# Kernel optimization log

Hardware: AMD Instinct MI355X
Metric: run time of the kernel (lower is better)

The kernel has to match this reference:

```python
import jax, jax.numpy as jnp
import numpy as np

N = 50000      # node_num
C = 64         # num_classes
G = 3          # number of metapath graphs (len(g))
E = 1200000    # edges per metapath graph
L = 2          # layers (PLPConv propagation steps)
D = 256        # input feature dim (feat_dims[0])
H = 256        # hidden_dim


def setup_inputs() -> dict:
    key = jax.random.key(0)
    ks = jax.random.split(key, 13)
    features0 = jax.random.normal(ks[0], (N, D), jnp.float32)
    labels = jax.random.randint(ks[1], (N,), 0, C)
    labels_one_hot = jax.nn.one_hot(labels, C, dtype=jnp.float32)
    # label_init: soft labels, rows on the simplex
    label_init = jax.nn.softmax(jax.random.normal(ks[2], (N, C), jnp.float32), axis=-1)
    train_mask = (jax.random.uniform(ks[3], (N, 1)) < 0.5).astype(jnp.float32)
    src = jax.random.randint(ks[4], (G, E), 0, N, dtype=jnp.int32)
    dst = jax.random.randint(ks[5], (G, E), 0, N, dtype=jnp.int32)
    # per-layer, per-graph learned edge logits (xavier-ish small init)
    e_edges = 0.1 * jax.random.normal(ks[6], (L, G, E), jnp.float32)
    attention = 0.5 * jax.random.normal(ks[7], (N, G), jnp.float32)
    alpha = 0.5 * jax.random.normal(ks[8], (N, 1), jnp.float32)
    W1 = jax.random.normal(ks[9], (D, H), jnp.float32) / np.sqrt(D)
    b1 = jnp.zeros((H,), jnp.float32)
    W2 = jax.random.normal(ks[10], (H, C), jnp.float32) / np.sqrt(H)
    b2 = jnp.zeros((C,), jnp.float32)
    return {"features0": features0, "label_init": label_init,
            "labels_one_hot": labels_one_hot, "train_mask": train_mask,
            "src": src, "dst": dst, "e_edges": e_edges,
            "attention": attention, "alpha": alpha,
            "W1": W1, "b1": b1, "W2": W2, "b2": b2}


def _edge_softmax(e, dst, n):
    # softmax of per-edge scalar over incoming edges of each dst node
    m = jax.ops.segment_max(e, dst, num_segments=n)
    a = jnp.exp(e - m[dst])
    s = jax.ops.segment_sum(a, dst, num_segments=n)
    return a / s[dst]


def reference(features0, label_init, labels_one_hot, train_mask,
              src, dst, e_edges, attention, alpha, W1, b1, W2, b2):
    n = label_init.shape[0]
    masked_label = 1.0 - train_mask            # (~masked).float(), [N,1]
    masked_oh = labels_one_hot * train_mask    # labels_one_hot * masked, [N,C]

    # Label propagation over each metapath graph (PLPConv stack, activation=None)
    h_prime = []
    for i in range(G):
        h = label_init
        for l in range(L):
            a = _edge_softmax(e_edges[l, i], dst[i], n)         # [E]
            msg = h[src[i]] * a[:, None]                        # gather-mul [E,C]
            h = jax.ops.segment_sum(msg, dst[i], num_segments=n)  # scatter-sum [N,C]
            h = h * masked_label + masked_oh                    # clamp train labels
        h_prime.append(h)
    x = jnp.stack(h_prime, axis=-1)                             # [N,C,G]

    att_mp = jax.nn.softmax(attention, axis=1)                  # [N,G]
    logits_lp = jnp.einsum('ncg,ng->nc', x, att_mp)             # [N,C]

    # MLP2 (2 layers, dropout=0): relu(x W1 + b1) W2 + b2
    hm = jax.nn.relu(features0 @ W1 + b1)
    logits_ns = hm @ W2 + b2                                    # [N,C]

    logits = jax.nn.sigmoid(alpha) * logits_lp + jax.nn.sigmoid(-alpha) * logits_ns
    return (logits, logits_lp, logits_ns)
```

## Files before the change

kernel.cpp:

```cpp
#include <hip/hip_runtime.h>
#include <hip/hip_bf16.h>

#define NN 50000
#define CC 64
#define GG 3
#define EE 1200000
#define LL 2
#define DD 256
#define HH 256
#define NB 196
#define NBLK 293
#define NBK (GG * NB)
#define BKCAP 8192


__device__ __forceinline__ ushort f2bf(float f) {
    unsigned b = __float_as_uint(f);
    return (ushort)((b + 0x7fffu + ((b >> 16) & 1u)) >> 16);
}
__device__ __forceinline__ float bf2f(unsigned u) {
    return __uint_as_float(u << 16);
}

typedef __attribute__((ext_vector_type(8))) short s8v;
typedef __attribute__((ext_vector_type(4))) float f4v;

template<int NWM, int NWN, bool A_FP32, bool OUT_RELU_BF16>
__global__ __launch_bounds__(256) void mfma_gemm_kernel(
    const void* __restrict__ Av, const ushort* __restrict__ Bt,
    const float* __restrict__ bias, void* __restrict__ Cv, int M, int Nc)
{
    static_assert(NWM * NWN == 4, "4 waves per block");
    const int tid = threadIdx.x;
    const int w = tid >> 6;
    const int l = tid & 63;
    const int wm = w / NWN;
    const int wn = w % NWN;
    const int r0 = blockIdx.x * (NWM * 64) + wm * 64;
    const int c0 = blockIdx.y * (NWN * 64) + wn * 64;
    const int lrow = l & 15;
    const int lk = (l >> 4) << 3;

    f4v acc[4][4] = {};

    for (int k0 = 0; k0 < 256; k0 += 32) {
        s8v a[4], b[4];
        #pragma unroll
        for (int i = 0; i < 4; i++) {
            int row = r0 + lrow + 16 * i;
            row = (row < M) ? row : (M - 1);
            if constexpr (A_FP32) {
                const float* Af = (const float*)Av;
                const float4* p = (const float4*)(Af + (size_t)row * 256 + k0 + lk);
                float4 f0 = p[0], f1 = p[1];
                union { ushort u[8]; s8v v; } t;
                t.u[0] = f2bf(f0.x); t.u[1] = f2bf(f0.y);
                t.u[2] = f2bf(f0.z); t.u[3] = f2bf(f0.w);
                t.u[4] = f2bf(f1.x); t.u[5] = f2bf(f1.y);
                t.u[6] = f2bf(f1.z); t.u[7] = f2bf(f1.w);
                a[i] = t.v;
            } else {
                const ushort* Ab = (const ushort*)Av;
                a[i] = *(const s8v*)(Ab + (size_t)row * 256 + k0 + lk);
            }
        }
        #pragma unroll
        for (int j = 0; j < 4; j++) {
            int col = c0 + lrow + 16 * j;
            b[j] = *(const s8v*)(Bt + (size_t)col * 256 + k0 + lk);
        }
        #pragma unroll
        for (int i = 0; i < 4; i++)
            #pragma unroll
            for (int j = 0; j < 4; j++)
                acc[i][j] = __builtin_amdgcn_mfma_f32_16x16x32_bf16(
                    a[i], b[j], acc[i][j], 0, 0, 0);
    }

    #pragma unroll
    for (int i = 0; i < 4; i++) {
        #pragma unroll
        for (int r = 0; r < 4; r++) {
            int row = r0 + 16 * i + (l >> 4) * 4 + r;
            if (row >= M) continue;
            #pragma unroll
            for (int j = 0; j < 4; j++) {
                int col = c0 + 16 * j + lrow;
                float v = acc[i][j][r] + bias[col];
                if constexpr (OUT_RELU_BF16) {
                    v = fmaxf(v, 0.f);
                    ((ushort*)Cv)[(size_t)row * Nc + col] = f2bf(v);
                } else {
                    ((float*)Cv)[(size_t)row * Nc + col] = v;
                }
            }
        }
    }
}

__global__ void wcvt_kernel(const float* __restrict__ W1,
                            const float* __restrict__ W2,
                            ushort* __restrict__ Wt1, ushort* __restrict__ Wt2)
{
    int idx = blockIdx.x * 256 + threadIdx.x;
    if (idx < 256 * 256) {
        int n = idx >> 8, k = idx & 255;
        Wt1[idx] = f2bf(W1[k * 256 + n]);
    } else {
        int i = idx - 256 * 256;
        if (i < 64 * 256) {
            int n = i >> 8, k = i & 255;
            Wt2[i] = f2bf(W2[k * 64 + n]);
        }
    }
}

__global__ void cvt_kernel(const float* __restrict__ in, ushort* __restrict__ out, int n4)
{
    int i = blockIdx.x * blockDim.x + threadIdx.x;
    if (i >= n4) return;
    float4 f = ((const float4*)in)[i];
    ushort4 u;
    u.x = f2bf(f.x); u.y = f2bf(f.y); u.z = f2bf(f.z); u.w = f2bf(f.w);
    ((ushort4*)out)[i] = u;
}

__global__ __launch_bounds__(256) void bhist_kernel(
    const int* __restrict__ dst, int* __restrict__ bcnt)
{
    int blk = blockIdx.x;
    int g = blk / NBLK;
    int bi = blk - g * NBLK;
    int base = bi * 4096;
    __shared__ int cnt[NB];
    int t = threadIdx.x;
    if (t < NB) cnt[t] = 0;
    __syncthreads();
    #pragma unroll
    for (int k = 0; k < 16; k++) {
        int e = base + k * 256 + t;
        if (e < EE) atomicAdd(&cnt[dst[g * EE + e] >> 8], 1);
    }
    __syncthreads();
    if (t < NB && cnt[t] > 0) atomicAdd(&bcnt[g * NB + t], cnt[t]);
}

__global__ void scan_bucket(const int* __restrict__ bcnt, int* __restrict__ bs)
{
    __shared__ int sd[256];
    __shared__ int s_run;
    int t = threadIdx.x;
    if (t == 0) s_run = 0;
    __syncthreads();
    for (int base = 0; base < NBK; base += 256) {
        int i = base + t;
        int v = (i < NBK) ? bcnt[i] : 0;
        sd[t] = v;
        __syncthreads();
        for (int o = 1; o < 256; o <<= 1) {
            int x = (t >= o) ? sd[t - o] : 0;
            __syncthreads();
            sd[t] += x;
            __syncthreads();
        }
        int run = s_run;
        __syncthreads();
        if (i < NBK) bs[i] = run + sd[t] - v;
        if (t == 255) s_run = run + sd[255];
        __syncthreads();
    }
    if (t == 0) bs[NBK] = GG * EE;
}

__global__ __launch_bounds__(256) void binA_kernel(
    const int* __restrict__ dst, const int* __restrict__ src,
    const float* __restrict__ e_edges, const int* __restrict__ bucket_start,
    int* __restrict__ fill, uint2* __restrict__ staging)
{
    int blk = blockIdx.x;
    int g = blk / NBLK;
    int bi = blk - g * NBLK;
    int base = bi * 4096;
    __shared__ int cnt[NB];
    __shared__ int cur[NB];
    __shared__ int rbase[NB];
    int t = threadIdx.x;
    if (t < NB) cnt[t] = 0;
    __syncthreads();

    int myd[16];
    #pragma unroll
    for (int k = 0; k < 16; k++) {
        int e = base + k * 256 + t;
        int d = (e < EE) ? dst[g * EE + e] : -1;
        myd[k] = d;
        if (d >= 0) atomicAdd(&cnt[d >> 8], 1);
    }
    __syncthreads();
    if (t < NB) {
        int c = cnt[t];
        int b = (c > 0) ? atomicAdd(&fill[g * NB + t], c) : 0;
        rbase[t] = bucket_start[g * NB + t];
        cur[t] = b;
    }
    __syncthreads();
    #pragma unroll
    for (int k = 0; k < 16; k++) {
        int d = myd[k];
        if (d >= 0) {
            int e = base + k * 256 + t;
            int bucket = d >> 8;
            int pos = rbase[bucket] + atomicAdd(&cur[bucket], 1);
            int idxg = g * EE + e;
            uint2 rec;
            rec.x = ((unsigned)f2bf(e_edges[idxg]) << 16) |
                    (unsigned)f2bf(e_edges[(size_t)(GG + g) * EE + e]);
            rec.y = ((unsigned)src[idxg] << 16) | (unsigned)(d & 255);
            staging[pos] = rec;
        }
    }
}

__global__ __launch_bounds__(1024) void bucket_kernel(
    const uint2* __restrict__ staging, const int* __restrict__ bucket_start,
    int* __restrict__ row_start, unsigned* __restrict__ packed0,
    unsigned* __restrict__ packed1)
{
    int blk = blockIdx.x;
    int g = blk / NB;
    int bucket = blk - g * NB;
    int bn = bucket << 8;
    int bnodes = min(256, NN - bn);
    int sbase = bucket_start[blk];
    int n = bucket_start[blk + 1] - sbase;
    int segStart = sbase - g * EE;
    const uint2* st = staging + sbase;

    __shared__ int hist[256];
    __shared__ int sd[256];
    __shared__ int cur[256];
    __shared__ float sm[512];
    __shared__ ushort ab0[BKCAP];
    __shared__ ushort ab1[BKCAP];
    __shared__ ushort sb[BKCAP];
    int t = threadIdx.x;
    if (t < 256) hist[t] = 0;
    if (t < 512) sm[t] = 0.f;
    __syncthreads();

    for (int i = t; i < n; i += 1024) {
        uint2 r = st[i];
        int dl = r.y & 0xff;
        atomicAdd(&hist[dl], 1);
        atomicAdd(&sm[dl], __expf(bf2f(r.x >> 16)));
        atomicAdd(&sm[256 + dl], __expf(bf2f(r.x & 0xffffu)));
    }
    __syncthreads();

    if (t < 256) sd[t] = hist[t];
    __syncthreads();
    for (int o = 1; o < 256; o <<= 1) {
        int x = (t < 256 && t >= o) ? sd[t - o] : 0;
        __syncthreads();
        if (t < 256) sd[t] += x;
        __syncthreads();
    }
    if (t < 256) {
        cur[t] = sd[t] - hist[t];
        if (t < bnodes)
            row_start[(size_t)g * (NN + 1) + bn + t] = segStart + sd[t] - hist[t];
        if (hist[t] > 0) {
            sm[t] = 1.f / sm[t];
            sm[256 + t] = 1.f / sm[256 + t];
        }
    }
    if (bucket == NB - 1 && t == 0) row_start[(size_t)g * (NN + 1) + NN] = EE;
    __syncthreads();

    for (int i = t; i < n; i += 1024) {
        uint2 r = st[i];
        int dl = r.y & 0xff;
        int pos = atomicAdd(&cur[dl], 1);
        ab0[pos] = f2bf(__expf(bf2f(r.x >> 16)) * sm[dl]);
        ab1[pos] = f2bf(__expf(bf2f(r.x & 0xffffu)) * sm[256 + dl]);
        sb[pos] = (ushort)(r.y >> 16);
    }
    __syncthreads();

    for (int i = t; i < n; i += 1024) {
        unsigned s = sb[i];
        packed0[(size_t)sbase + i] = ((unsigned)ab0[i] << 16) | s;
        packed1[(size_t)sbase + i] = ((unsigned)ab1[i] << 16) | s;
    }
}

__device__ __forceinline__ void consume8(unsigned packed, int cnt,
                                         const ushort* __restrict__ tab,
                                         int lane, float& acc)
{
    for (int k0 = 0; k0 < cnt; k0 += 8) {
        unsigned pk[8];
        #pragma unroll
        for (int u = 0; u < 8; u++) pk[u] = __shfl(packed, k0 + u);
        float vals[8];
        #pragma unroll
        for (int u = 0; u < 8; u++)
            vals[u] = bf2f((unsigned)tab[(size_t)(pk[u] & 0xffffu) * 64 + lane]);
        #pragma unroll
        for (int u = 0; u < 8; u++)
            acc = fmaf(vals[u], __uint_as_float(pk[u] & 0xffff0000u), acc);
    }
}

__global__ __launch_bounds__(256) void prop0_kernel(
    const ushort* __restrict__ lab_bf, const float* __restrict__ labels_oh,
    const float* __restrict__ train_mask, const int* __restrict__ row_start,
    const unsigned* __restrict__ packed0, ushort* __restrict__ h_buf)
{
    int wid = (blockIdx.x * blockDim.x + threadIdx.x) >> 6;
    int lane = threadIdx.x & 63;
    if (wid >= GG * NN) return;
    int g = wid / NN;
    int v = wid - g * NN;
    const int* rs = row_start + (size_t)g * (NN + 1);
    int s = rs[v], tE = rs[v + 1];
    const unsigned* pk = packed0 + (size_t)g * EE;

    float acc = 0.f;
    for (int base = s; base < tE; base += 64) {
        int j = base + lane;
        unsigned packed = (j < tE) ? pk[j] : 0u;
        int cnt = min(64, tE - base);
        consume8(packed, cnt, lab_bf, lane, acc);
    }
    float tm = train_mask[v];
    float res = acc * (1.f - tm) + labels_oh[(size_t)v * 64 + lane] * tm;
    h_buf[(size_t)wid * 64 + lane] = f2bf(res);
}

__global__ __launch_bounds__(256) void final_kernel(
    const ushort* __restrict__ h_buf, const float* __restrict__ labels_oh,
    const float* __restrict__ train_mask, const float* __restrict__ attention,
    const float* __restrict__ alpha, const int* __restrict__ row_start,
    const unsigned* __restrict__ packed1, const float* __restrict__ out_ns,
    float* __restrict__ out_logits, float* __restrict__ out_lp)
{
    int wid = (blockIdx.x * blockDim.x + threadIdx.x) >> 6;
    int lane = threadIdx.x & 63;
    if (wid >= NN) return;
    int v = wid;
    float tm = train_mask[v];
    float ml = 1.f - tm;
    float moh = labels_oh[(size_t)v * 64 + lane] * tm;
    float a0 = attention[v * 3], a1 = attention[v * 3 + 1], a2 = attention[v * 3 + 2];
    float mxa = fmaxf(a0, fmaxf(a1, a2));
    float e0 = __expf(a0 - mxa), e1 = __expf(a1 - mxa), e2 = __expf(a2 - mxa);
    float ainv = 1.f / (e0 + e1 + e2);
    float attw[3] = {e0 * ainv, e1 * ainv, e2 * ainv};
    float lp = 0.f;
    #pragma unroll
    for (int g = 0; g < GG; g++) {
        const int* rs = row_start + (size_t)g * (NN + 1);
        int s = rs[v], tE = rs[v + 1];
        const unsigned* pk = packed1 + (size_t)g * EE;
        const ushort* hin = h_buf + (size_t)g * NN * 64;

        float acc = 0.f;
        for (int base = s; base < tE; base += 64) {
            int j = base + lane;
            unsigned packed = (j < tE) ? pk[j] : 0u;
            int cnt = min(64, tE - base);
            consume8(packed, cnt, hin, lane, acc);
        }
        float hf = acc * ml + moh;
        lp += attw[g] * hf;
    }
    size_t o = (size_t)v * 64 + lane;
    out_lp[o] = lp;
    float al = alpha[v];
    float sg = 1.f / (1.f + __expf(-al));
    out_logits[o] = sg * lp + (1.f - sg) * out_ns[o];
}

extern "C" void kernel_launch(void* const* d_in, const int* in_sizes, int n_in,
                              void* d_out, int out_size, void* d_ws, size_t ws_size,
                              hipStream_t stream)
{
    const float* features0  = (const float*)d_in[0];
    const float* label_init = (const float*)d_in[1];
    const float* labels_oh  = (const float*)d_in[2];
    const float* train_mask = (const float*)d_in[3];
    const int*   src        = (const int*)d_in[4];
    const int*   dst        = (const int*)d_in[5];
    const float* e_edges    = (const float*)d_in[6];
    const float* attention  = (const float*)d_in[7];
    const float* alpha      = (const float*)d_in[8];
    const float* W1         = (const float*)d_in[9];
    const float* b1         = (const float*)d_in[10];
    const float* W2         = (const float*)d_in[11];
    const float* b2         = (const float*)d_in[12];

    float* out        = (float*)d_out;
    float* out_logits = out;
    float* out_lp     = out + (size_t)NN * CC;
    float* out_ns     = out + 2 * (size_t)NN * CC;

    char* base = (char*)d_ws;
    size_t off = 0;
    auto alloc = [&](size_t bytes) -> void* {
        void* p = base + off;
        off = (off + bytes + 255) & ~(size_t)255;
        return p;
    };
    int*      bcnt         = (int*)alloc((size_t)NBK * sizeof(int));
    int*      fill         = (int*)alloc((size_t)NBK * sizeof(int));
    size_t    zero_bytes   = off;
    int*      bucket_start = (int*)alloc((size_t)(NBK + 1) * sizeof(int));
    int*      row_start    = (int*)alloc((size_t)GG * (NN + 1) * sizeof(int));
    uint2*    staging      = (uint2*)alloc((size_t)GG * EE * sizeof(uint2));
    unsigned* packed0      = (unsigned*)alloc((size_t)GG * EE * sizeof(unsigned));
    unsigned* packed1      = (unsigned*)alloc((size_t)GG * EE * sizeof(unsigned));
    ushort*   h_buf        = (ushort*)alloc((size_t)GG * NN * CC * sizeof(ushort));
    ushort*   lab_bf       = (ushort*)alloc((size_t)NN * CC * sizeof(ushort));

    ushort* Wt1   = (ushort*)packed0;
    ushort* Wt2   = Wt1 + 256 * 256;
    ushort* hm_bf = (ushort*)staging;

    wcvt_kernel<<<(256 * 256 + 64 * 256) / 256, 256, 0, stream>>>(W1, W2, Wt1, Wt2);
    mfma_gemm_kernel<2, 2, true, true><<<dim3((NN + 127) / 128, 2), 256, 0, stream>>>(
        features0, Wt1, b1, hm_bf, NN, HH);
    mfma_gemm_kernel<4, 1, false, false><<<dim3((NN + 255) / 256, 1), 256, 0, stream>>>(
        hm_bf, Wt2, b2, out_ns, NN, CC);

    cvt_kernel<<<(NN * CC / 4 + 255) / 256, 256, 0, stream>>>(
        label_init, lab_bf, NN * CC / 4);

    hipMemsetAsync(bcnt, 0, zero_bytes, stream);
    bhist_kernel<<<GG * NBLK, 256, 0, stream>>>(dst, bcnt);
    scan_bucket<<<1, 256, 0, stream>>>(bcnt, bucket_start);
    binA_kernel<<<GG * NBLK, 256, 0, stream>>>(
        dst, src, e_edges, bucket_start, fill, staging);
    bucket_kernel<<<GG * NB, 1024, 0, stream>>>(
        staging, bucket_start, row_start, packed0, packed1);

    prop0_kernel<<<((size_t)GG * NN * 64 + 255) / 256, 256, 0, stream>>>(
        lab_bf, labels_oh, train_mask, row_start, packed0, h_buf);

    final_kernel<<<((size_t)NN * 64 + 255) / 256, 256, 0, stream>>>(
        h_buf, labels_oh, train_mask, attention, alpha, row_start, packed1,
        out_ns, out_logits, out_lp);
}
```

Before: 529.8 us.

## Stage binned edge records in LDS before coalesced bucket writes

The binning kernel now handles 16K edges per 1024-thread block. It sorts the edge records locally in shared memory using a per-block prefix scan over bucket counts, then writes each bucket's contiguous run to global staging with wave-cooperative coalesced stores. The aim is to replace the scattered 8-byte global writes with runs of contiguous writes. In exchange it uses 128KB of LDS per block and much fewer blocks (222), which limits occupancy and adds extra synchronisation for the scan.

```diff
diff --git a/kernel.cpp b/kernel.cpp
--- a/kernel.cpp
+++ b/kernel.cpp
@@ -12,6 +12,8 @@
 #define NBLK 293
 #define NBK (GG * NB)
 #define BKCAP 8192
+#define CH 16384
+#define CBLK 74
 
 
 __device__ __forceinline__ ushort f2bf(float f) {
@@ -172,18 +174,21 @@
     if (t == 0) bs[NBK] = GG * EE;
 }
 
-__global__ __launch_bounds__(256) void binA_kernel(
+__global__ __launch_bounds__(1024) void binA_kernel(
     const int* __restrict__ dst, const int* __restrict__ src,
     const float* __restrict__ e_edges, const int* __restrict__ bucket_start,
     int* __restrict__ fill, uint2* __restrict__ staging)
 {
     int blk = blockIdx.x;
-    int g = blk / NBLK;
-    int bi = blk - g * NBLK;
-    int base = bi * 4096;
+    int g = blk / CBLK;
+    int bi = blk - g * CBLK;
+    int base = bi * CH;
+    __shared__ uint2 rec[CH];
     __shared__ int cnt[NB];
+    __shared__ int lstart[NB];
     __shared__ int cur[NB];
-    __shared__ int rbase[NB];
+    __shared__ int gbase[NB];
+    __shared__ int sd[256];
     int t = threadIdx.x;
     if (t < NB) cnt[t] = 0;
     __syncthreads();
@@ -191,33 +196,53 @@
     int myd[16];
     #pragma unroll
     for (int k = 0; k < 16; k++) {
-        int e = base + k * 256 + t;
+        int e = base + k * 1024 + t;
         int d = (e < EE) ? dst[g * EE + e] : -1;
         myd[k] = d;
         if (d >= 0) atomicAdd(&cnt[d >> 8], 1);
     }
     __syncthreads();
+
+    if (t < 256) sd[t] = (t < NB) ? cnt[t] : 0;
+    __syncthreads();
+    for (int o = 1; o < 256; o <<= 1) {
+        int x = (t < 256 && t >= o) ? sd[t - o] : 0;
+        __syncthreads();
+        if (t < 256) sd[t] += x;
+        __syncthreads();
+    }
     if (t < NB) {
         int c = cnt[t];
-        int b = (c > 0) ? atomicAdd(&fill[g * NB + t], c) : 0;
-        rbase[t] = bucket_start[g * NB + t];
-        cur[t] = b;
-    }
-    __syncthreads();
+        int ls = sd[t] - c;
+        lstart[t] = ls;
+        cur[t] = ls;
+        int fo = (c > 0) ? atomicAdd(&fill[g * NB + t], c) : 0;
+        gbase[t] = bucket_start[g * NB + t] + fo;
+    }
+    __syncthreads();
+
     #pragma unroll
     for (int k = 0; k < 16; k++) {
         int d = myd[k];
         if (d >= 0) {
-            int e = base + k * 256 + t;
-            int bucket = d >> 8;
-            int pos = rbase[bucket] + atomicAdd(&cur[bucket], 1);
+            int e = base + k * 1024 + t;
+            int pos = atomicAdd(&cur[d >> 8], 1);
             int idxg = g * EE + e;
-            uint2 rec;
-            rec.x = ((unsigned)f2bf(e_edges[idxg]) << 16) |
-                    (unsigned)f2bf(e_edges[(size_t)(GG + g) * EE + e]);
-            rec.y = ((unsigned)src[idxg] << 16) | (unsigned)(d & 255);
-            staging[pos] = rec;
-        }
+            uint2 r;
+            r.x = ((unsigned)f2bf(e_edges[idxg]) << 16) |
+                  (unsigned)f2bf(e_edges[(size_t)(GG + g) * EE + e]);
+            r.y = ((unsigned)src[idxg] << 16) | (unsigned)(d & 255);
+            rec[pos] = r;
+        }
+    }
+    __syncthreads();
+
+    int w = t >> 6, lane = t & 63;
+    for (int b = w; b < NB; b += 16) {
+        int c = cnt[b];
+        int ls = lstart[b];
+        uint2* dp = staging + gbase[b];
+        for (int i = lane; i < c; i += 64) dp[i] = rec[ls + i];
     }
 }
 
@@ -439,7 +464,7 @@
     hipMemsetAsync(bcnt, 0, zero_bytes, stream);
     bhist_kernel<<<GG * NBLK, 256, 0, stream>>>(dst, bcnt);
     scan_bucket<<<1, 256, 0, stream>>>(bcnt, bucket_start);
-    binA_kernel<<<GG * NBLK, 256, 0, stream>>>(
+    binA_kernel<<<GG * CBLK, 1024, 0, stream>>>(
         dst, src, e_edges, bucket_start, fill, staging);
     bucket_kernel<<<GG * NB, 1024, 0, stream>>>(
         staging, bucket_start, row_start, packed0, packed1);
```

New measurement: 482.9 us. -8.8%, faster.
